# Optimization experiments

Hardware: AMD Instinct MI355X
Metric: run time of the kernel (lower is better)

Reference implementation:

```python
import jax, jax.numpy as jnp
import numpy as np

H, W = 64, 64
SCALE = 0.75
PF = 4                      # pupil_padding_factor (hard-coded in module)
PAD = int(0.5 * (PF - 1) * H)  # 96 per side -> padded grid 256x256


def _pupil_buffers():
    us = jnp.linspace(-1.0, 1.0, H) / SCALE
    vs = jnp.linspace(-1.0, 1.0, W) / SCALE
    US, VS = jnp.meshgrid(us, vs, indexing='ij')
    R = jnp.sqrt(US ** 2 + VS ** 2)
    pupil_magnitude = (R <= 1.0).astype(jnp.float32)          # apod=False
    pupil_prop = jnp.sqrt(1.0 - jnp.minimum(R, 1.0) ** 2)
    kx = jnp.fft.fftshift(jnp.fft.fftfreq(H * PF)).astype(jnp.float32)
    ky = jnp.fft.fftshift(jnp.fft.fftfreq(W * PF)).astype(jnp.float32)
    KX, KY = jnp.meshgrid(kx, ky, indexing='ij')
    return pupil_magnitude, pupil_prop, KX, KY


def setup_inputs() -> dict:
    key = jax.random.key(0)
    ks = jax.random.split(key, 7)
    B, N = 64, 4
    return {
        'x': jax.random.normal(ks[0], (B, N, 1, 1), jnp.float32) * 8.0,   # pixel shifts
        'y': jax.random.normal(ks[1], (B, N, 1, 1), jnp.float32) * 8.0,
        'z': jax.random.normal(ks[2], (B, N, 1, 1), jnp.float32) * 2.0,
        'A': jax.random.uniform(ks[3], (B, N, 1, 1), jnp.float32, 0.5, 2.0),
        'bg': jax.random.uniform(ks[4], (B, N, 1, 1), jnp.float32, 0.0, 0.1),
        'p': jax.random.uniform(ks[5], (B, N, 1, 1), jnp.float32),
        'pupil_phase': jax.random.normal(ks[6], (H, W), jnp.float32) * 0.1,  # xavier-ish init
    }


def reference(x, y, z, A, bg, p, pupil_phase):
    mag, prop, KX, KY = _pupil_buffers()
    two_pi = 2.0 * np.pi
    mag_p = jnp.pad(mag, PAD)                      # [4H,4W]
    prop_p = jnp.pad(prop, PAD)                    # [4H,4W]
    phase_p = jnp.pad(pupil_phase, PAD)[None, None]  # [1,1,4H,4W]
    # per-emitter phase ramps (lateral shift) + defocus term -> [B,N,4H,4W]
    phase = (phase_p
             - two_pi * KX[None, None] * x
             - two_pi * KY[None, None] * y
             + prop_p[None, None] * z)
    pupil = mag_p[None, None] * jnp.exp(1j * phase)  # complex64 [B,N,4H,4W]
    field = jnp.fft.ifft2(jnp.fft.ifftshift(pupil, axes=(-2, -1)))
    psf = jnp.fft.ifftshift(jnp.real(field * jnp.conj(field)), axes=(-2, -1))
    psf = psf / jnp.max(psf, axis=(-2, -1), keepdims=True)
    psf = psf[:, :, PAD:-PAD, PAD:-PAD]            # crop back to [B,N,H,W]
    img = psf * A + bg
    img = img * (p > 0.5)
    return img.sum(axis=1, keepdims=True)          # [B,1,H,W]
```

## Files before the change

kernel.cpp:

```cpp
#include <hip/hip_runtime.h>

#define NSUB 48
#define J0   8
#define PIF  3.14159265358979323846f

#define R4BFLY(B0r,B0i,B1r,B1i,B2r,B2i,B3r,B3i, A0r,A0i,A1r,A1i,A2r,A2i,A3r,A3i) \
  { float c0r=(B0r)+(B2r), c0i=(B0i)+(B2i), d0r=(B0r)-(B2r), d0i=(B0i)-(B2i);     \
    float c1r=(B1r)+(B3r), c1i=(B1i)+(B3i), d1r=(B1r)-(B3r), d1i=(B1i)-(B3i);     \
    A0r=c0r+c1r; A0i=c0i+c1i; A2r=c0r-c1r; A2i=c0i-c1i;                           \
    A1r=d0r-d1i; A1i=d0i+d1r; A3r=d0r+d1i; A3i=d0i-d1r; }

__device__ __forceinline__ void build_tw_P(
    int tid, float x, float y, float z,
    const float* __restrict__ phase_in,
    float2* __restrict__ tw, float2* __restrict__ P2k)
{
    {
        float s, c;
        __sincosf((float)tid * (PIF / 128.0f), &s, &c);
        tw[tid] = make_float2(c, s);
    }
    const float c1 = PIF / 128.0f;
    for (int idx = tid; idx < NSUB * NSUB; idx += 256) {
        int jj = idx / NSUB;
        int kk = idx - jj * NSUB;
        int j = jj + J0, k = kk + J0;
        float us = ((float)(2 * j) * (1.0f / 63.0f) - 1.0f) * (4.0f / 3.0f);
        float vs = ((float)(2 * k) * (1.0f / 63.0f) - 1.0f) * (4.0f / 3.0f);
        float r2 = us * us + vs * vs;
        float re = 0.0f, im = 0.0f;
        if (r2 <= 1.0f) {
            float prop = sqrtf(fmaxf(1.0f - r2, 0.0f));
            float ph = phase_in[j * 64 + k] + prop * z
                       - c1 * ((float)(j - 32) * x + (float)(k - 32) * y);
            float s, c;
            __sincosf(ph, &s, &c);
            re = c; im = s;
        }
        P2k[kk * 49 + jj] = make_float2(re, im);
    }
}

__global__ __launch_bounds__(256, 4)
void psf_max_kernel(const float* __restrict__ X, const float* __restrict__ Y,
                    const float* __restrict__ Z,
                    const float* __restrict__ phase_in,
                    float* __restrict__ maxws, float* __restrict__ stash,
                    int do_stash)
{
    __shared__ float2 tw[256];
    __shared__ __align__(16) float2 PG[NSUB * 66];
    __shared__ float red[4];

    const int tid = threadIdx.x;
    const int pair = blockIdx.x >> 2;
    const int rres = blockIdx.x & 3;
    const float x = X[pair], y = Y[pair], z = Z[pair];

    build_tw_P(tid, x, y, z, phase_in, tw, PG);
    __syncthreads();

    const int jj = tid % 48;
    const int vg = tid / 48;
    float GqR[4][4], GqI[4][4];
    if (tid < 192) {
        _Pragma("unroll")
        for (int p = 0; p < 4; ++p) {
            const int vb = rres + 4 * (vg * 4 + p);
            float2 w0 = tw[(J0 * vb) & 255];
            float2 st = tw[vb];
            float wr = w0.x, wi = w0.y;
            const float cr = st.x, ci = st.y;
            float Cr[4] = {0,0,0,0}, Ci[4] = {0,0,0,0};
#define GBODY(KK, S) do {                                                         \
            float2 pv = PG[(KK) * 49 + jj];                                       \
            Cr[S] = fmaf(pv.x, wr, fmaf(-pv.y, wi, Cr[S]));                       \
            Ci[S] = fmaf(pv.x, wi, fmaf( pv.y, wr, Ci[S]));                       \
            float t  = wi * ci;                                                   \
            float nr = fmaf(wr, cr, -t);                                          \
            float ni = fmaf(wr, ci, wi * cr);                                     \
            wr = nr; wi = ni; } while (0)
            #pragma unroll 1
            for (int kk = 0; kk < NSUB; kk += 4) {
                GBODY(kk + 0, 0); GBODY(kk + 1, 1); GBODY(kk + 2, 2); GBODY(kk + 3, 3);
            }
#undef GBODY
            R4BFLY(Cr[0],Ci[0], Cr[1],Ci[1], Cr[2],Ci[2], Cr[3],Ci[3],
                   GqR[p][0],GqI[p][0], GqR[p][1],GqI[p][1],
                   GqR[p][2],GqI[p][2], GqR[p][3],GqI[p][3]);
        }
    }
    __syncthreads();
    if (tid < 192) {
        _Pragma("unroll")
        for (int p = 0; p < 4; ++p) {
            _Pragma("unroll")
            for (int q = 0; q < 4; ++q)
                PG[jj * 66 + (vg * 4 + p) + 16 * q] = make_float2(GqR[p][q], GqI[p][q]);
        }
    }
    __syncthreads();

    const int lane = tid & 63;
    const int wv = tid >> 6;
    const float2 w0l = tw[(8 * lane) & 255];
    const float2 stl = tw[lane];
    const float crr = stl.x, cii = stl.y;
    float lmax = 0.0f;
    #pragma unroll 1
    for (int p = 0; p < 4; ++p) {
        const int vloc0 = wv * 16 + 4 * p;
        const int vb = vloc0;
        float Br[4][4], Bi[4][4];
        _Pragma("unroll")
        for (int s = 0; s < 4; ++s) {
            _Pragma("unroll")
            for (int vv = 0; vv < 4; ++vv) { Br[s][vv] = 0.0f; Bi[s][vv] = 0.0f; }
        }
        float wr = w0l.x, wi = w0l.y;
#define FBODY(JJ, S) do {                                                         \
        const float4 g01 = *(const float4*)&PG[(JJ) * 66 + vb];                   \
        const float4 g23 = *(const float4*)&PG[(JJ) * 66 + vb + 2];               \
        Br[S][0] = fmaf(g01.x, wr, fmaf(-g01.y, wi, Br[S][0]));                   \
        Bi[S][0] = fmaf(g01.x, wi, fmaf( g01.y, wr, Bi[S][0]));                   \
        Br[S][1] = fmaf(g01.z, wr, fmaf(-g01.w, wi, Br[S][1]));                   \
        Bi[S][1] = fmaf(g01.z, wi, fmaf( g01.w, wr, Bi[S][1]));                   \
        Br[S][2] = fmaf(g23.x, wr, fmaf(-g23.y, wi, Br[S][2]));                   \
        Bi[S][2] = fmaf(g23.x, wi, fmaf( g23.y, wr, Bi[S][2]));                   \
        Br[S][3] = fmaf(g23.z, wr, fmaf(-g23.w, wi, Br[S][3]));                   \
        Bi[S][3] = fmaf(g23.z, wi, fmaf( g23.w, wr, Bi[S][3]));                   \
        float t  = wi * cii;                                                      \
        float nr = fmaf(wr, crr, -t);                                             \
        float ni = fmaf(wr, cii, wi * crr);                                       \
        wr = nr; wi = ni; } while (0)
        #pragma unroll 1
        for (int j4 = 0; j4 < NSUB; j4 += 4) {
            FBODY(j4 + 0, 0); FBODY(j4 + 1, 1); FBODY(j4 + 2, 2); FBODY(j4 + 3, 3);
        }
#undef FBODY
        const bool cropcol = (vloc0 < 8) | (vloc0 >= 56);
        _Pragma("unroll")
        for (int vv = 0; vv < 4; ++vv) {
            float a0r,a0i,a1r,a1i,a2r,a2i,a3r,a3i;
            R4BFLY(Br[0][vv],Bi[0][vv], Br[1][vv],Bi[1][vv],
                   Br[2][vv],Bi[2][vv], Br[3][vv],Bi[3][vv],
                   a0r,a0i, a1r,a1i, a2r,a2i, a3r,a3i);
            float m0 = fmaf(a0r, a0r, a0i * a0i);
            float m1 = fmaf(a1r, a1r, a1i * a1i);
            float m2 = fmaf(a2r, a2r, a2i * a2i);
            float m3 = fmaf(a3r, a3r, a3i * a3i);
            lmax = fmaxf(lmax, fmaxf(fmaxf(m0, m1), fmaxf(m2, m3)));
            if (do_stash && cropcol) {
                int c = ((rres + 4 * (vloc0 + vv)) + 32) & 255;
                float mc = (lane < 32) ? m0 : m3;
                stash[pair * 4096 + ((lane ^ 32) << 6) + c] = mc;
            }
        }
    }

    for (int off = 32; off > 0; off >>= 1)
        lmax = fmaxf(lmax, __shfl_down(lmax, off, 64));
    if ((tid & 63) == 0) red[tid >> 6] = lmax;
    __syncthreads();
    if (tid == 0) {
        float m = fmaxf(fmaxf(red[0], red[1]), fmaxf(red[2], red[3]));
        atomicMax((unsigned int*)&maxws[pair], __float_as_uint(m));
    }
}

__global__ __launch_bounds__(256)
void combine_kernel(const float* __restrict__ Aamp, const float* __restrict__ BG,
                    const float* __restrict__ Pmask,
                    const float* __restrict__ maxws, const float* __restrict__ stash,
                    float* __restrict__ out)
{
    const int b = blockIdx.x >> 2;
    const int base = (blockIdx.x & 3) * 1024 + threadIdx.x * 4;
    float4 acc = make_float4(0.f, 0.f, 0.f, 0.f);
    float bgtot = 0.0f;
    #pragma unroll
    for (int n = 0; n < 4; ++n) {
        const int pair = b * 4 + n;
        if (Pmask[pair] > 0.5f) {
            const float s = Aamp[pair] / maxws[pair];
            bgtot += BG[pair];
            const float4 v = *(const float4*)(stash + pair * 4096 + base);
            acc.x = fmaf(v.x, s, acc.x);
            acc.y = fmaf(v.y, s, acc.y);
            acc.z = fmaf(v.z, s, acc.z);
            acc.w = fmaf(v.w, s, acc.w);
        }
    }
    *(float4*)(out + b * 4096 + base) =
        make_float4(acc.x + bgtot, acc.y + bgtot, acc.z + bgtot, acc.w + bgtot);
}

__global__ __launch_bounds__(256, 4)
void psf_crop_kernel(const float* __restrict__ X, const float* __restrict__ Y,
                     const float* __restrict__ Z, const float* __restrict__ Aamp,
                     const float* __restrict__ BG, const float* __restrict__ Pmask,
                     const float* __restrict__ phase_in,
                     const float* __restrict__ maxws,
                     float* __restrict__ out)
{
    const int pair = blockIdx.x >> 2;
    const int vblk = blockIdx.x & 3;
    if (Pmask[pair] <= 0.5f) return;

    __shared__ float2 tw[256];
    __shared__ __align__(16) float2 PG[NSUB * 49];

    const int tid = threadIdx.x;
    const float x = X[pair], y = Y[pair], z = Z[pair];
    build_tw_P(tid, x, y, z, phase_in, tw, PG);
    __syncthreads();

    const int jj = tid % 48;
    const int vg = tid / 48;
    float gr4[4], gi4[4], gwr[4], gwi[4], gcr[4], gci[4];
    if (tid < 192) {
        _Pragma("unroll")
        for (int c = 0; c < 4; ++c) {
            int acol = vblk * 16 + vg * 4 + c;
            int v = (acol + 224) & 255;
            float2 w0 = tw[(J0 * v) & 255];
            float2 st = tw[v];
            gwr[c] = w0.x; gwi[c] = w0.y; gcr[c] = st.x; gci[c] = st.y;
            gr4[c] = 0.0f; gi4[c] = 0.0f;
        }
        #pragma unroll 4
        for (int kk = 0; kk < NSUB; ++kk) {
            float2 pv = PG[kk * 49 + jj];
            _Pragma("unroll")
            for (int c = 0; c < 4; ++c) {
                gr4[c] = fmaf(pv.x, gwr[c], fmaf(-pv.y, gwi[c], gr4[c]));
                gi4[c] = fmaf(pv.x, gwi[c], fmaf( pv.y, gwr[c], gi4[c]));
                float t  = gwi[c] * gci[c];
                float nr = fmaf(gwr[c], gcr[c], -t);
                float ni = fmaf(gwr[c], gci[c], gwi[c] * gcr[c]);
                gwr[c] = nr; gwi[c] = ni;
            }
        }
    }
    __syncthreads();
    if (tid < 192) {
        _Pragma("unroll")
        for (int c = 0; c < 4; ++c)
            PG[jj * 18 + vg * 4 + c] = make_float2(gr4[c], gi4[c]);
    }
    __syncthreads();

    const float scale = Aamp[pair] / maxws[pair];
    const float bgv = BG[pair];

    const int lane = tid & 63;
    const int wv = tid >> 6;
    const int u = (lane + 224) & 255;
    const float2 w0l = tw[(8 * u) & 255];
    const float2 stl = tw[u];
    const float crr = stl.x, cii = stl.y;
    const int vb = wv * 4;
    float ar[4], ai[4];
    _Pragma("unroll")
    for (int c = 0; c < 4; ++c) { ar[c] = 0.0f; ai[c] = 0.0f; }
    float wr = w0l.x, wi = w0l.y;
    #pragma unroll 4
    for (int j = 0; j < NSUB; ++j) {
        const float4 g01 = *(const float4*)&PG[j * 18 + vb];
        const float4 g23 = *(const float4*)&PG[j * 18 + vb + 2];
        ar[0] = fmaf(g01.x, wr, fmaf(-g01.y, wi, ar[0]));
        ai[0] = fmaf(g01.x, wi, fmaf( g01.y, wr, ai[0]));
        ar[1] = fmaf(g01.z, wr, fmaf(-g01.w, wi, ar[1]));
        ai[1] = fmaf(g01.z, wi, fmaf( g01.w, wr, ai[1]));
        ar[2] = fmaf(g23.x, wr, fmaf(-g23.y, wi, ar[2]));
        ai[2] = fmaf(g23.x, wi, fmaf( g23.y, wr, ai[2]));
        ar[3] = fmaf(g23.z, wr, fmaf(-g23.w, wi, ar[3]));
        ai[3] = fmaf(g23.z, wi, fmaf( g23.w, wr, ai[3]));
        float t  = wi * cii;
        float nr = fmaf(wr, crr, -t);
        float ni = fmaf(wr, cii, wi * crr);
        wr = nr; wi = ni;
    }

    float* outb = out + ((pair >> 2) << 12) + lane * 64 + vblk * 16 + vb;
    _Pragma("unroll")
    for (int c = 0; c < 4; ++c) {
        float m = fmaf(ar[c], ar[c], ai[c] * ai[c]);
        atomicAdd(&outb[c], fmaf(m, scale, bgv));
    }
}

extern "C" void kernel_launch(void* const* d_in, const int* in_sizes, int n_in,
                              void* d_out, int out_size, void* d_ws, size_t ws_size,
                              hipStream_t stream)
{
    const float* x  = (const float*)d_in[0];
    const float* y  = (const float*)d_in[1];
    const float* z  = (const float*)d_in[2];
    const float* A  = (const float*)d_in[3];
    const float* bg = (const float*)d_in[4];
    const float* p  = (const float*)d_in[5];
    const float* ph = (const float*)d_in[6];
    float* out = (float*)d_out;
    float* maxws = (float*)d_ws;
    float* stash = maxws + 256;

    const size_t need = 256u * sizeof(float) + 256u * 4096u * sizeof(float);
    const int do_stash = (ws_size >= need) ? 1 : 0;

    hipMemsetAsync(d_ws, 0, 256 * sizeof(float), stream);

    hipLaunchKernelGGL(psf_max_kernel, dim3(1024), dim3(256), 0, stream,
                       x, y, z, ph, maxws, stash, do_stash);
    if (do_stash) {
        hipLaunchKernelGGL(combine_kernel, dim3(256), dim3(256), 0, stream,
                           A, bg, p, maxws, stash, out);
    } else {
        hipMemsetAsync(d_out, 0, (size_t)out_size * sizeof(float), stream);
        hipLaunchKernelGGL(psf_crop_kernel, dim3(1024), dim3(256), 0, stream,
                           x, y, z, A, bg, p, ph, maxws, out);
    }
}
```

Measured before the change: 107.1 us.

## Restructure DFT stages with shared-twiddle radix-4 and radix-8 row factorization

The first (column) DFT stage now accumulates four strided subsums per output using a shared twiddle recurrence across the four p outputs, then applies per-output twiddles and a radix-4 butterfly. This reuses each loaded pupil value across all four outputs instead of reloading it. The second stage switches from radix-4 with 64 lanes to radix-8 with 32 lanes, so the serial DFT length is halved at the cost of more accumulator registers. The per-pair atomicMax plus memset is replaced by per-block max writes that the consumers reduce, removing one memset launch and the atomics.

```diff
diff --git a/kernel.cpp b/kernel.cpp
--- a/kernel.cpp
+++ b/kernel.cpp
@@ -3,6 +3,7 @@
 #define NSUB 48
 #define J0   8
 #define PIF  3.14159265358979323846f
+#define C8   0.70710678118654752440f
 
 #define R4BFLY(B0r,B0i,B1r,B1i,B2r,B2i,B3r,B3i, A0r,A0i,A1r,A1i,A2r,A2i,A3r,A3i) \
   { float c0r=(B0r)+(B2r), c0i=(B0i)+(B2i), d0r=(B0r)-(B2r), d0i=(B0i)-(B2i);     \
@@ -45,7 +46,7 @@
 void psf_max_kernel(const float* __restrict__ X, const float* __restrict__ Y,
                     const float* __restrict__ Z,
                     const float* __restrict__ phase_in,
-                    float* __restrict__ maxws, float* __restrict__ stash,
+                    float* __restrict__ maxws4, float* __restrict__ stash,
                     int do_stash)
 {
     __shared__ float2 tw[256];
@@ -62,98 +63,137 @@
 
     const int jj = tid % 48;
     const int vg = tid / 48;
-    float GqR[4][4], GqI[4][4];
+    float GBr[4][4], GBi[4][4];
     if (tid < 192) {
+        float gwr[4], gwi[4], gsr[4], gsi[4];
         _Pragma("unroll")
         for (int p = 0; p < 4; ++p) {
-            const int vb = rres + 4 * (vg * 4 + p);
-            float2 w0 = tw[(J0 * vb) & 255];
-            float2 st = tw[vb];
-            float wr = w0.x, wi = w0.y;
-            const float cr = st.x, ci = st.y;
-            float Cr[4] = {0,0,0,0}, Ci[4] = {0,0,0,0};
-#define GBODY(KK, S) do {                                                         \
-            float2 pv = PG[(KK) * 49 + jj];                                       \
-            Cr[S] = fmaf(pv.x, wr, fmaf(-pv.y, wi, Cr[S]));                       \
-            Ci[S] = fmaf(pv.x, wi, fmaf( pv.y, wr, Ci[S]));                       \
-            float t  = wi * ci;                                                   \
-            float nr = fmaf(wr, cr, -t);                                          \
-            float ni = fmaf(wr, ci, wi * cr);                                     \
-            wr = nr; wi = ni; } while (0)
-            #pragma unroll 1
-            for (int kk = 0; kk < NSUB; kk += 4) {
-                GBODY(kk + 0, 0); GBODY(kk + 1, 1); GBODY(kk + 2, 2); GBODY(kk + 3, 3);
+            const int v = rres + 4 * (vg * 4 + p);
+            float2 st = tw[(4 * v) & 255];
+            gsr[p] = st.x; gsi[p] = st.y;
+            gwr[p] = 1.0f; gwi[p] = 0.0f;
+            _Pragma("unroll")
+            for (int s = 0; s < 4; ++s) { GBr[p][s] = 0.0f; GBi[p][s] = 0.0f; }
+        }
+        #pragma unroll 2
+        for (int m = 0; m < 12; ++m) {
+            const float2 p0 = PG[(4 * m + 0) * 49 + jj];
+            const float2 p1 = PG[(4 * m + 1) * 49 + jj];
+            const float2 p2 = PG[(4 * m + 2) * 49 + jj];
+            const float2 p3 = PG[(4 * m + 3) * 49 + jj];
+            _Pragma("unroll")
+            for (int p = 0; p < 4; ++p) {
+                const float wr = gwr[p], wi = gwi[p];
+                GBr[p][0] = fmaf(p0.x, wr, fmaf(-p0.y, wi, GBr[p][0]));
+                GBi[p][0] = fmaf(p0.x, wi, fmaf( p0.y, wr, GBi[p][0]));
+                GBr[p][1] = fmaf(p1.x, wr, fmaf(-p1.y, wi, GBr[p][1]));
+                GBi[p][1] = fmaf(p1.x, wi, fmaf( p1.y, wr, GBi[p][1]));
+                GBr[p][2] = fmaf(p2.x, wr, fmaf(-p2.y, wi, GBr[p][2]));
+                GBi[p][2] = fmaf(p2.x, wi, fmaf( p2.y, wr, GBi[p][2]));
+                GBr[p][3] = fmaf(p3.x, wr, fmaf(-p3.y, wi, GBr[p][3]));
+                GBi[p][3] = fmaf(p3.x, wi, fmaf( p3.y, wr, GBi[p][3]));
+                float t  = wi * gsi[p];
+                gwr[p] = fmaf(wr, gsr[p], -t);
+                gwi[p] = fmaf(wr, gsi[p], wi * gsr[p]);
             }
-#undef GBODY
-            R4BFLY(Cr[0],Ci[0], Cr[1],Ci[1], Cr[2],Ci[2], Cr[3],Ci[3],
-                   GqR[p][0],GqI[p][0], GqR[p][1],GqI[p][1],
-                   GqR[p][2],GqI[p][2], GqR[p][3],GqI[p][3]);
         }
     }
     __syncthreads();
     if (tid < 192) {
         _Pragma("unroll")
         for (int p = 0; p < 4; ++p) {
-            _Pragma("unroll")
-            for (int q = 0; q < 4; ++q)
-                PG[jj * 66 + (vg * 4 + p) + 16 * q] = make_float2(GqR[p][q], GqI[p][q]);
-        }
-    }
-    __syncthreads();
-
-    const int lane = tid & 63;
-    const int wv = tid >> 6;
-    const float2 w0l = tw[(8 * lane) & 255];
-    const float2 stl = tw[lane];
+            const int m = vg * 4 + p;
+            const int v = rres + 4 * m;
+            float Tr[4], Ti[4];
+            _Pragma("unroll")
+            for (int s = 0; s < 4; ++s) {
+                float2 u = tw[((s + 8) * v) & 255];
+                Tr[s] = GBr[p][s] * u.x - GBi[p][s] * u.y;
+                Ti[s] = GBr[p][s] * u.y + GBi[p][s] * u.x;
+            }
+            float A0r,A0i,A1r,A1i,A2r,A2i,A3r,A3i;
+            R4BFLY(Tr[0],Ti[0], Tr[1],Ti[1], Tr[2],Ti[2], Tr[3],Ti[3],
+                   A0r,A0i, A1r,A1i, A2r,A2i, A3r,A3i);
+            PG[jj * 66 + m +  0] = make_float2(A0r, A0i);
+            PG[jj * 66 + m + 16] = make_float2(A1r, A1i);
+            PG[jj * 66 + m + 32] = make_float2(A2r, A2i);
+            PG[jj * 66 + m + 48] = make_float2(A3r, A3i);
+        }
+    }
+    __syncthreads();
+
+    const int ub = tid & 31;
+    const int vgrp = tid >> 5;
+    const float2 w0l = tw[(8 * ub) & 255];
+    const float2 stl = tw[ub];
     const float crr = stl.x, cii = stl.y;
     float lmax = 0.0f;
     #pragma unroll 1
-    for (int p = 0; p < 4; ++p) {
-        const int vloc0 = wv * 16 + 4 * p;
-        const int vb = vloc0;
-        float Br[4][4], Bi[4][4];
-        _Pragma("unroll")
-        for (int s = 0; s < 4; ++s) {
-            _Pragma("unroll")
-            for (int vv = 0; vv < 4; ++vv) { Br[s][vv] = 0.0f; Bi[s][vv] = 0.0f; }
+    for (int c2 = 0; c2 < 2; ++c2) {
+        const int vb = vgrp * 8 + c2 * 4;
+        float FBr[8][4], FBi[8][4];
+        _Pragma("unroll")
+        for (int s = 0; s < 8; ++s) {
+            _Pragma("unroll")
+            for (int vv = 0; vv < 4; ++vv) { FBr[s][vv] = 0.0f; FBi[s][vv] = 0.0f; }
         }
         float wr = w0l.x, wi = w0l.y;
 #define FBODY(JJ, S) do {                                                         \
         const float4 g01 = *(const float4*)&PG[(JJ) * 66 + vb];                   \
         const float4 g23 = *(const float4*)&PG[(JJ) * 66 + vb + 2];               \
-        Br[S][0] = fmaf(g01.x, wr, fmaf(-g01.y, wi, Br[S][0]));                   \
-        Bi[S][0] = fmaf(g01.x, wi, fmaf( g01.y, wr, Bi[S][0]));                   \
-        Br[S][1] = fmaf(g01.z, wr, fmaf(-g01.w, wi, Br[S][1]));                   \
-        Bi[S][1] = fmaf(g01.z, wi, fmaf( g01.w, wr, Bi[S][1]));                   \
-        Br[S][2] = fmaf(g23.x, wr, fmaf(-g23.y, wi, Br[S][2]));                   \
-        Bi[S][2] = fmaf(g23.x, wi, fmaf( g23.y, wr, Bi[S][2]));                   \
-        Br[S][3] = fmaf(g23.z, wr, fmaf(-g23.w, wi, Br[S][3]));                   \
-        Bi[S][3] = fmaf(g23.z, wi, fmaf( g23.w, wr, Bi[S][3]));                   \
+        FBr[S][0] = fmaf(g01.x, wr, fmaf(-g01.y, wi, FBr[S][0]));                 \
+        FBi[S][0] = fmaf(g01.x, wi, fmaf( g01.y, wr, FBi[S][0]));                 \
+        FBr[S][1] = fmaf(g01.z, wr, fmaf(-g01.w, wi, FBr[S][1]));                 \
+        FBi[S][1] = fmaf(g01.z, wi, fmaf( g01.w, wr, FBi[S][1]));                 \
+        FBr[S][2] = fmaf(g23.x, wr, fmaf(-g23.y, wi, FBr[S][2]));                 \
+        FBi[S][2] = fmaf(g23.x, wi, fmaf( g23.y, wr, FBi[S][2]));                 \
+        FBr[S][3] = fmaf(g23.z, wr, fmaf(-g23.w, wi, FBr[S][3]));                 \
+        FBi[S][3] = fmaf(g23.z, wi, fmaf( g23.w, wr, FBi[S][3]));                 \
         float t  = wi * cii;                                                      \
         float nr = fmaf(wr, crr, -t);                                             \
         float ni = fmaf(wr, cii, wi * crr);                                       \
         wr = nr; wi = ni; } while (0)
         #pragma unroll 1
-        for (int j4 = 0; j4 < NSUB; j4 += 4) {
-            FBODY(j4 + 0, 0); FBODY(j4 + 1, 1); FBODY(j4 + 2, 2); FBODY(j4 + 3, 3);
+        for (int j8 = 0; j8 < NSUB; j8 += 8) {
+            FBODY(j8 + 0, 0); FBODY(j8 + 1, 1); FBODY(j8 + 2, 2); FBODY(j8 + 3, 3);
+            FBODY(j8 + 4, 4); FBODY(j8 + 5, 5); FBODY(j8 + 6, 6); FBODY(j8 + 7, 7);
         }
 #undef FBODY
-        const bool cropcol = (vloc0 < 8) | (vloc0 >= 56);
+        const bool cropcol = (vb < 8) | (vb >= 56);
         _Pragma("unroll")
         for (int vv = 0; vv < 4; ++vv) {
-            float a0r,a0i,a1r,a1i,a2r,a2i,a3r,a3i;
-            R4BFLY(Br[0][vv],Bi[0][vv], Br[1][vv],Bi[1][vv],
-                   Br[2][vv],Bi[2][vv], Br[3][vv],Bi[3][vv],
-                   a0r,a0i, a1r,a1i, a2r,a2i, a3r,a3i);
-            float m0 = fmaf(a0r, a0r, a0i * a0i);
-            float m1 = fmaf(a1r, a1r, a1i * a1i);
-            float m2 = fmaf(a2r, a2r, a2i * a2i);
-            float m3 = fmaf(a3r, a3r, a3i * a3i);
-            lmax = fmaxf(lmax, fmaxf(fmaxf(m0, m1), fmaxf(m2, m3)));
+            float E0r,E0i,E1r,E1i,E2r,E2i,E3r,E3i;
+            float O0r,O0i,O1r,O1i,O2r,O2i,O3r,O3i;
+            R4BFLY(FBr[0][vv],FBi[0][vv], FBr[2][vv],FBi[2][vv],
+                   FBr[4][vv],FBi[4][vv], FBr[6][vv],FBi[6][vv],
+                   E0r,E0i, E1r,E1i, E2r,E2i, E3r,E3i);
+            R4BFLY(FBr[1][vv],FBi[1][vv], FBr[3][vv],FBi[3][vv],
+                   FBr[5][vv],FBi[5][vv], FBr[7][vv],FBi[7][vv],
+                   O0r,O0i, O1r,O1i, O2r,O2i, O3r,O3i);
+            float F0r = E0r + O0r, F0i = E0i + O0i;
+            float F4r = E0r - O0r, F4i = E0i - O0i;
+            float F2r = E2r - O2i, F2i = E2i + O2r;
+            float F6r = E2r + O2i, F6i = E2i - O2r;
+            float p1r = C8 * (O1r - O1i), p1i = C8 * (O1r + O1i);
+            float F1r = E1r + p1r, F1i = E1i + p1i;
+            float F5r = E1r - p1r, F5i = E1i - p1i;
+            float q3r = -C8 * (O3r + O3i), q3i = C8 * (O3r - O3i);
+            float F3r = E3r + q3r, F3i = E3i + q3i;
+            float F7r = E3r - q3r, F7i = E3i - q3i;
+            float m0 = fmaf(F0r, F0r, F0i * F0i);
+            float m1 = fmaf(F1r, F1r, F1i * F1i);
+            float m2 = fmaf(F2r, F2r, F2i * F2i);
+            float m3 = fmaf(F3r, F3r, F3i * F3i);
+            float m4 = fmaf(F4r, F4r, F4i * F4i);
+            float m5 = fmaf(F5r, F5r, F5i * F5i);
+            float m6 = fmaf(F6r, F6r, F6i * F6i);
+            float m7 = fmaf(F7r, F7r, F7i * F7i);
+            lmax = fmaxf(lmax, fmaxf(fmaxf(fmaxf(m0, m1), fmaxf(m2, m3)),
+                                     fmaxf(fmaxf(m4, m5), fmaxf(m6, m7))));
             if (do_stash && cropcol) {
-                int c = ((rres + 4 * (vloc0 + vv)) + 32) & 255;
-                float mc = (lane < 32) ? m0 : m3;
-                stash[pair * 4096 + ((lane ^ 32) << 6) + c] = mc;
+                const int c = ((rres + 4 * (vb + vv)) + 32) & 255;
+                stash[pair * 4096 + ((ub + 32) << 6) + c] = m0;
+                stash[pair * 4096 + (ub << 6) + c] = m7;
             }
         }
     }
@@ -163,15 +203,14 @@
     if ((tid & 63) == 0) red[tid >> 6] = lmax;
     __syncthreads();
     if (tid == 0) {
-        float m = fmaxf(fmaxf(red[0], red[1]), fmaxf(red[2], red[3]));
-        atomicMax((unsigned int*)&maxws[pair], __float_as_uint(m));
+        maxws4[blockIdx.x] = fmaxf(fmaxf(red[0], red[1]), fmaxf(red[2], red[3]));
     }
 }
 
 __global__ __launch_bounds__(256)
 void combine_kernel(const float* __restrict__ Aamp, const float* __restrict__ BG,
                     const float* __restrict__ Pmask,
-                    const float* __restrict__ maxws, const float* __restrict__ stash,
+                    const float* __restrict__ maxws4, const float* __restrict__ stash,
                     float* __restrict__ out)
 {
     const int b = blockIdx.x >> 2;
@@ -182,7 +221,9 @@
     for (int n = 0; n < 4; ++n) {
         const int pair = b * 4 + n;
         if (Pmask[pair] > 0.5f) {
-            const float s = Aamp[pair] / maxws[pair];
+            const float4 m4 = *(const float4*)&maxws4[pair * 4];
+            const float mx = fmaxf(fmaxf(m4.x, m4.y), fmaxf(m4.z, m4.w));
+            const float s = Aamp[pair] / mx;
             bgtot += BG[pair];
             const float4 v = *(const float4*)(stash + pair * 4096 + base);
             acc.x = fmaf(v.x, s, acc.x);
@@ -200,7 +241,7 @@
                      const float* __restrict__ Z, const float* __restrict__ Aamp,
                      const float* __restrict__ BG, const float* __restrict__ Pmask,
                      const float* __restrict__ phase_in,
-                     const float* __restrict__ maxws,
+                     const float* __restrict__ maxws4,
                      float* __restrict__ out)
 {
     const int pair = blockIdx.x >> 2;
@@ -250,7 +291,9 @@
     }
     __syncthreads();
 
-    const float scale = Aamp[pair] / maxws[pair];
+    const float4 m4 = *(const float4*)&maxws4[pair * 4];
+    const float mx = fmaxf(fmaxf(m4.x, m4.y), fmaxf(m4.z, m4.w));
+    const float scale = Aamp[pair] / mx;
     const float bgv = BG[pair];
 
     const int lane = tid & 63;
@@ -302,22 +345,20 @@
     const float* p  = (const float*)d_in[5];
     const float* ph = (const float*)d_in[6];
     float* out = (float*)d_out;
-    float* maxws = (float*)d_ws;
-    float* stash = maxws + 256;
-
-    const size_t need = 256u * sizeof(float) + 256u * 4096u * sizeof(float);
+    float* maxws4 = (float*)d_ws;
+    float* stash  = maxws4 + 1024;
+
+    const size_t need = 1024u * sizeof(float) + 256u * 4096u * sizeof(float);
     const int do_stash = (ws_size >= need) ? 1 : 0;
 
-    hipMemsetAsync(d_ws, 0, 256 * sizeof(float), stream);
-
     hipLaunchKernelGGL(psf_max_kernel, dim3(1024), dim3(256), 0, stream,
-                       x, y, z, ph, maxws, stash, do_stash);
+                       x, y, z, ph, maxws4, stash, do_stash);
     if (do_stash) {
         hipLaunchKernelGGL(combine_kernel, dim3(256), dim3(256), 0, stream,
-                           A, bg, p, maxws, stash, out);
+                           A, bg, p, maxws4, stash, out);
     } else {
         hipMemsetAsync(d_out, 0, (size_t)out_size * sizeof(float), stream);
         hipLaunchKernelGGL(psf_crop_kernel, dim3(1024), dim3(256), 0, stream,
-                           x, y, z, A, bg, p, ph, maxws, out);
-    }
-}
+                           x, y, z, A, bg, p, ph, maxws4, out);
+    }
+}
```

After: 95.36 us. 1.12x faster.
